# Kernel optimization log

Measured on AMD Instinct MI355X. Metric: run time of the kernel, lower is better.

The kernel has to match this reference:

```python
import jax, jax.numpy as jnp
import numpy as np

N_NODES = 100000
N_EDGES = 640000
LATDIM = 128
GNN_LAYER = 3
LN_EPS = 1e-5


def setup_inputs() -> dict:
    key = jax.random.key(0)
    k1, k2, k3, k4 = jax.random.split(key, 4)
    embeds = jax.random.normal(k1, (N_NODES, LATDIM), dtype=jnp.float32)
    adj_row = jax.random.randint(k2, (N_EDGES,), 0, N_NODES, dtype=jnp.int32)
    adj_col = jax.random.randint(k3, (N_EDGES,), 0, N_NODES, dtype=jnp.int32)
    adj_val = jax.random.uniform(k4, (N_EDGES,), dtype=jnp.float32)
    return {"embeds": embeds, "adj_row": adj_row, "adj_col": adj_col, "adj_val": adj_val}


def _layer_norm(x):
    # nn.LayerNorm(latdim, elementwise_affine=False)
    mu = jnp.mean(x, axis=-1, keepdims=True)
    var = jnp.mean(jnp.square(x - mu), axis=-1, keepdims=True)
    return (x - mu) / jnp.sqrt(var + LN_EPS)


def _spmm(adj_row, adj_col, adj_val, x):
    # out[r] += val * x[c] for each edge (r, c, val)  -- sparse [N,N] @ [N,d]
    msgs = adj_val[:, None] * x[adj_col]  # [E, d]
    return jax.ops.segment_sum(msgs, adj_row, num_segments=N_NODES)


def reference(embeds, adj_row, adj_col, adj_val):
    x = _layer_norm(embeds)
    acc = jnp.zeros_like(x)  # gnn_layer > 0, so hop-0 embeds are NOT included
    for _ in range(GNN_LAYER):
        x = _spmm(adj_row, adj_col, adj_val, x)
        acc = acc + x
    return acc
```

## Files before the change

### kernel.cpp

```cpp
#include <hip/hip_runtime.h>

#define N_NODES 100000
#define N_EDGES 640000
#define LATDIM  128
#define LN_EPS  1e-5f

typedef unsigned int u32;
typedef float f32x4 __attribute__((ext_vector_type(4)));
typedef float f32x2 __attribute__((ext_vector_type(2)));

#define SCAN_NB   98
#define N_PAD     (SCAN_NB * 1024)

#define LN_BLOCKS   (N_NODES / 8)

#define CNT_BLOCKS  100
#define CNT_K       25

#define APP_K      7
#define APP_EDGES  (256 * APP_K)
#define APP_NB     ((N_EDGES + APP_EDGES - 1) / APP_EDGES)

__device__ __forceinline__ float bflo(u32 u) { return __uint_as_float(u << 16); }
__device__ __forceinline__ float bfhi(u32 u) { return __uint_as_float(u & 0xffff0000u); }
__device__ __forceinline__ u32 pack_bf2(float a, float b) {
    u32 ua = __float_as_uint(a), ub = __float_as_uint(b);
    ua = (ua + 0x7fffu + ((ua >> 16) & 1u)) >> 16;
    ub = (ub + 0x7fffu + ((ub >> 16) & 1u)) >> 16;
    return ua | (ub << 16);
}

__device__ __forceinline__ u32 pack_edge(int col, float val) {
    u32 q = (u32)fminf(val * 32768.0f + 0.5f, 32767.0f);
    return (u32)col | (q << 17);
}
__device__ __forceinline__ int   edge_col(u32 r) { return (int)(r & 0x1FFFFu); }
__device__ __forceinline__ float edge_val(u32 r) { return (float)(r >> 17) * (1.0f / 32768.0f); }

__global__ __launch_bounds__(256) void ln_count_kernel(const float* __restrict__ in,
                                                       u32* __restrict__ out,
                                                       const int* __restrict__ rowi,
                                                       int* __restrict__ partials) {
    int b = blockIdx.x;
    if (b >= CNT_BLOCKS) {
        int tid  = threadIdx.x;
        int wave = tid >> 6;
        int lane = tid & 63;
        int half = lane >> 5;
        int sub  = lane & 31;
        int row  = (b - CNT_BLOCKS) * 8 + wave * 2 + half;
        f32x4 v = __builtin_nontemporal_load(((const f32x4*)in) + (size_t)row * 32 + sub);
        float s  = v.x + v.y + v.z + v.w;
        float ss = v.x * v.x + v.y * v.y + v.z * v.z + v.w * v.w;
        #pragma unroll
        for (int o = 16; o > 0; o >>= 1) {
            s  += __shfl_xor(s,  o, 64);
            ss += __shfl_xor(ss, o, 64);
        }
        float mu   = s * (1.0f / LATDIM);
        float var  = ss * (1.0f / LATDIM) - mu * mu;
        float rstd = rsqrtf(var + LN_EPS);
        uint2 w;
        w.x = pack_bf2((v.x - mu) * rstd, (v.y - mu) * rstd);
        w.y = pack_bf2((v.z - mu) * rstd, (v.w - mu) * rstd);
        ((uint2*)out)[(size_t)row * 32 + sub] = w;
    } else {
        __shared__ int hist[SCAN_NB];
        int t = threadIdx.x;
        if (t < SCAN_NB) hist[t] = 0;
        __syncthreads();
        int e0 = b * (256 * CNT_K);
        #pragma unroll
        for (int k = 0; k < CNT_K; ++k) {
            int e = e0 + k * 256 + t;
            atomicAdd(&hist[rowi[e] >> 10], 1);
        }
        __syncthreads();
        if (t < SCAN_NB) partials[b * SCAN_NB + t] = hist[t];
    }
}

__global__ __launch_bounds__(128) void scan_chunks_kernel(const int* __restrict__ partials,
                                                          int* __restrict__ bsums,
                                                          int* __restrict__ gcur) {
    __shared__ int ss[128];
    int t = threadIdx.x;
    int own = 0;
    if (t < SCAN_NB) {
        for (int i = 0; i < CNT_BLOCKS; ++i) own += partials[i * SCAN_NB + t];
    }
    ss[t] = own;
    __syncthreads();
    #pragma unroll
    for (int o = 1; o < 128; o <<= 1) {
        int u = 0;
        if (t >= o) u = ss[t - o];
        __syncthreads();
        if (t >= o) ss[t] += u;
        __syncthreads();
    }
    if (t < SCAN_NB) {
        int off = ss[t] - own;
        bsums[t] = off;
        gcur[t]  = off;
    }
    if (t == SCAN_NB) bsums[SCAN_NB] = N_EDGES;
}

__global__ __launch_bounds__(256) void bucket_append_kernel(const int* __restrict__ rowi,
                                                            const int* __restrict__ coli,
                                                            const float* __restrict__ vali,
                                                            int* __restrict__ gcur,
                                                            uint2* __restrict__ staging) {
    __shared__ int hist[SCAN_NB];
    __shared__ int base[SCAN_NB];
    int t = threadIdx.x;
    if (t < SCAN_NB) hist[t] = 0;
    __syncthreads();
    int e0 = blockIdx.x * APP_EDGES;
    int r[APP_K]; int c[APP_K]; float v[APP_K]; int bk[APP_K];
    #pragma unroll
    for (int k = 0; k < APP_K; ++k) {
        int e = e0 + k * 256 + t;
        if (e < N_EDGES) {
            r[k] = rowi[e]; c[k] = coli[e]; v[k] = vali[e];
            bk[k] = r[k] >> 10;
            atomicAdd(&hist[bk[k]], 1);
        } else {
            bk[k] = -1;
        }
    }
    __syncthreads();
    if (t < SCAN_NB) {
        int h = hist[t];
        base[t] = h ? atomicAdd(&gcur[t], h) : 0;
        hist[t] = 0;
    }
    __syncthreads();
    #pragma unroll
    for (int k = 0; k < APP_K; ++k) {
        if (bk[k] >= 0) {
            int idx = atomicAdd(&hist[bk[k]], 1);
            staging[base[bk[k]] + idx] =
                make_uint2(((u32)(r[k] & 1023) << 17) | (u32)c[k],
                           __float_as_uint(v[k]));
        }
    }
}

__global__ __launch_bounds__(256) void fine_scatter_kernel(int* __restrict__ cnt,
                                                           const int* __restrict__ bsums,
                                                           const uint2* __restrict__ staging,
                                                           u32* __restrict__ recs) {
    __shared__ int cur[1024];
    __shared__ int ts[256];
    int b = blockIdx.x, t = threadIdx.x;
    *(int4*)&cur[t * 4] = make_int4(0, 0, 0, 0);
    __syncthreads();
    int gbase = bsums[b];
    int n = bsums[b + 1] - gbase;
    for (int i = t; i < n; i += 256) {
        uint2 s = staging[gbase + i];
        atomicAdd(&cur[s.x >> 17], 1);
    }
    __syncthreads();
    int4 v = *(const int4*)&cur[t * 4];
    int s = v.x + v.y + v.z + v.w;
    ts[t] = s;
    __syncthreads();
    #pragma unroll
    for (int o = 1; o < 256; o <<= 1) {
        int u = 0;
        if (t >= o) u = ts[t - o];
        __syncthreads();
        if (t >= o) ts[t] += u;
        __syncthreads();
    }
    int excl = ts[t] - s;
    int4 w;
    w.x = excl;
    w.y = excl + v.x;
    w.z = excl + v.x + v.y;
    w.w = excl + v.x + v.y + v.z;
    *(int4*)&cnt[b * 1024 + t * 4] = w;
    *(int4*)&cur[t * 4] = w;
    __syncthreads();
    for (int i = t; i < n; i += 256) {
        uint2 s2 = staging[gbase + i];
        int rowLocal = (int)(s2.x >> 17);
        int col = (int)(s2.x & 0x1FFFFu);
        int pos = gbase + atomicAdd(&cur[rowLocal], 1);
        recs[pos] = pack_edge(col, __uint_as_float(s2.y));
    }
}

__global__ __launch_bounds__(256) void spmm_csr_kernel(const int* __restrict__ cnt,
                                                       const int* __restrict__ bsums,
                                                       const u32* __restrict__ recs,
                                                       const u32* __restrict__ x,
                                                       u32* __restrict__ y,
                                                       const u32* __restrict__ add0,
                                                       const u32* __restrict__ add1,
                                                       float* __restrict__ out,
                                                       int mode) {
    int tid  = threadIdx.x;
    int wave = tid >> 6;
    int lane = tid & 63;
    int row  = blockIdx.x * 4 + wave;
    int e   = cnt[row]     + bsums[row >> 10];
    int end = cnt[row + 1] + bsums[(row + 1) >> 10];
    float a0 = 0.f, a1 = 0.f;
    for (; e + 4 <= end; e += 4) {
        u32 r0 = recs[e], r1 = recs[e+1], r2 = recs[e+2], r3 = recs[e+3];
        u32 g0 = x[(size_t)edge_col(r0) * 64 + lane];
        u32 g1 = x[(size_t)edge_col(r1) * 64 + lane];
        u32 g2 = x[(size_t)edge_col(r2) * 64 + lane];
        u32 g3 = x[(size_t)edge_col(r3) * 64 + lane];
        float v0 = edge_val(r0), v1 = edge_val(r1);
        float v2 = edge_val(r2), v3 = edge_val(r3);
        a0 += v0 * bflo(g0); a1 += v0 * bfhi(g0);
        a0 += v1 * bflo(g1); a1 += v1 * bfhi(g1);
        a0 += v2 * bflo(g2); a1 += v2 * bfhi(g2);
        a0 += v3 * bflo(g3); a1 += v3 * bfhi(g3);
    }
    if (e + 2 <= end) {
        u32 r0 = recs[e], r1 = recs[e+1];
        u32 g0 = x[(size_t)edge_col(r0) * 64 + lane];
        u32 g1 = x[(size_t)edge_col(r1) * 64 + lane];
        float v0 = edge_val(r0), v1 = edge_val(r1);
        a0 += v0 * bflo(g0); a1 += v0 * bfhi(g0);
        a0 += v1 * bflo(g1); a1 += v1 * bfhi(g1);
        e += 2;
    }
    if (e < end) {
        u32 r = recs[e];
        u32 g = x[(size_t)edge_col(r) * 64 + lane];
        float v = edge_val(r);
        a0 += v * bflo(g); a1 += v * bfhi(g);
    }
    size_t oi = (size_t)row * 64 + lane;
    if (mode == 2) {
        u32 b0 = add0[oi];
        u32 b1 = add1[oi];
        a0 += bflo(b0) + bflo(b1);
        a1 += bfhi(b0) + bfhi(b1);
        f32x2 q = {a0, a1};
        __builtin_nontemporal_store(q, ((f32x2*)(out + (size_t)row * LATDIM)) + lane);
    } else {
        y[oi] = pack_bf2(a0, a1);
    }
}

__global__ __launch_bounds__(256) void ln_f32_kernel(const float* __restrict__ in,
                                                     float* __restrict__ out) {
    int tid  = threadIdx.x;
    int wave = tid >> 6;
    int lane = tid & 63;
    int half = lane >> 5;
    int sub  = lane & 31;
    int row  = blockIdx.x * 8 + wave * 2 + half;
    if (row >= N_NODES) return;
    float4 v = ((const float4*)in)[(size_t)row * 32 + sub];
    float s  = v.x + v.y + v.z + v.w;
    float ss = v.x * v.x + v.y * v.y + v.z * v.z + v.w * v.w;
    #pragma unroll
    for (int o = 16; o > 0; o >>= 1) {
        s  += __shfl_xor(s,  o, 64);
        ss += __shfl_xor(ss, o, 64);
    }
    float mu   = s * (1.0f / LATDIM);
    float var  = ss * (1.0f / LATDIM) - mu * mu;
    float rstd = rsqrtf(var + LN_EPS);
    float4 o4;
    o4.x = (v.x - mu) * rstd; o4.y = (v.y - mu) * rstd;
    o4.z = (v.z - mu) * rstd; o4.w = (v.w - mu) * rstd;
    ((float4*)out)[(size_t)row * 32 + sub] = o4;
}

__global__ __launch_bounds__(256) void spmm_atomic_kernel(const int* __restrict__ rowi,
                                                          const int* __restrict__ coli,
                                                          const float* __restrict__ vali,
                                                          const float* __restrict__ x,
                                                          float* __restrict__ y) {
    int t = blockIdx.x * 256 + threadIdx.x;
    int e = t >> 5;
    if (e >= N_EDGES) return;
    int k = t & 31;
    int r = rowi[e];
    int c = coli[e];
    float v = vali[e];
    float4 xv = ((const float4*)(x + (size_t)c * LATDIM))[k];
    float* yp = y + (size_t)r * LATDIM + k * 4;
    atomicAdd(yp + 0, v * xv.x);
    atomicAdd(yp + 1, v * xv.y);
    atomicAdd(yp + 2, v * xv.z);
    atomicAdd(yp + 3, v * xv.w);
}

__global__ __launch_bounds__(256) void addz_kernel(float* __restrict__ acc,
                                                   const float* __restrict__ x,
                                                   float* __restrict__ z,
                                                   int first) {
    size_t i = (size_t)blockIdx.x * 256 + threadIdx.x;
    float4 xv = ((const float4*)x)[i];
    float4* ap = ((float4*)acc) + i;
    if (first) {
        *ap = xv;
    } else {
        float4 a = *ap;
        a.x += xv.x; a.y += xv.y; a.z += xv.z; a.w += xv.w;
        *ap = a;
    }
    if (z) ((float4*)z)[i] = make_float4(0.f, 0.f, 0.f, 0.f);
}

extern "C" void kernel_launch(void* const* d_in, const int* in_sizes, int n_in,
                              void* d_out, int out_size, void* d_ws, size_t ws_size,
                              hipStream_t stream) {
    const float* embeds  = (const float*)d_in[0];
    const int*   adj_row = (const int*)d_in[1];
    const int*   adj_col = (const int*)d_in[2];
    const float* adj_val = (const float*)d_in[3];
    float* out = (float*)d_out;

    u32*   A16   = (u32*)d_ws;
    u32*   B16   = A16 + (size_t)N_NODES * (LATDIM / 2);
    int*   cnt   = (int*)(B16 + (size_t)N_NODES * (LATDIM / 2));
    int*   partials = cnt + N_PAD;
    int*   bsums = partials + CNT_BLOCKS * SCAN_NB;
    int*   gcur  = bsums + 128;
    uint2* staging = (uint2*)(gcur + 128);
    u32*   recs  = (u32*)(staging + N_EDGES);
    size_t need  = (size_t)((char*)(recs + N_EDGES) - (char*)d_ws);

    const int rowGrid = N_NODES / 4;

    if (ws_size >= need) {
        ln_count_kernel<<<CNT_BLOCKS + LN_BLOCKS, 256, 0, stream>>>(embeds, A16,
                                                                    adj_row, partials);
        scan_chunks_kernel<<<1, 128, 0, stream>>>(partials, bsums, gcur);
        bucket_append_kernel<<<APP_NB, 256, 0, stream>>>(adj_row, adj_col, adj_val,
                                                         gcur, staging);
        fine_scatter_kernel<<<SCAN_NB, 256, 0, stream>>>(cnt, bsums, staging, recs);
        spmm_csr_kernel<<<rowGrid, 256, 0, stream>>>(cnt, bsums, recs, A16, B16,
                                                     nullptr, nullptr, nullptr, 0);
        spmm_csr_kernel<<<rowGrid, 256, 0, stream>>>(cnt, bsums, recs, B16, A16,
                                                     nullptr, nullptr, nullptr, 0);
        spmm_csr_kernel<<<rowGrid, 256, 0, stream>>>(cnt, bsums, recs, A16, nullptr,
                                                     B16, A16, out, 2);
    } else {
        float* A = (float*)d_ws;
        float* B = A + (size_t)N_NODES * LATDIM;
        const size_t rowBytes = (size_t)N_NODES * LATDIM * sizeof(float);
        const int spmmGrid = (N_EDGES * 32 + 255) / 256;
        const int addGrid  = (N_NODES * LATDIM / 4 + 255) / 256;
        ln_f32_kernel<<<LN_BLOCKS, 256, 0, stream>>>(embeds, A);
        hipMemsetAsync(B, 0, rowBytes, stream);
        spmm_atomic_kernel<<<spmmGrid, 256, 0, stream>>>(adj_row, adj_col, adj_val, A, B);
        addz_kernel<<<addGrid, 256, 0, stream>>>(out, B, A, 1);
        spmm_atomic_kernel<<<spmmGrid, 256, 0, stream>>>(adj_row, adj_col, adj_val, B, A);
        addz_kernel<<<addGrid, 256, 0, stream>>>(out, A, B, 0);
        spmm_atomic_kernel<<<spmmGrid, 256, 0, stream>>>(adj_row, adj_col, adj_val, A, B);
        addz_kernel<<<addGrid, 256, 0, stream>>>(out, B, nullptr, 0);
    }
}
```

Before: 261.6 us.

## Process two adjacent CSR rows per 16-lane group with 16-byte gathers

The SpMM kernel now gives each 16-lane group a pair of consecutive rows, walking their combined edge range once and splitting each edge's weight between the two rows' accumulators by comparing the edge index to the row boundary. Each lane gathers a uint4 (8 bf16 values) instead of one u32, so every gathered row becomes a single 256-byte load by 16 lanes. The dequantisation scale is moved out of the loop and applied once at the end. This cuts per-edge instruction overhead and divergence from short rows, at the cost of doubled FMAs (half of them multiply by zero) and higher register pressure from 16 accumulators.

New measurement: 242.2 us. 1.08x faster.

```diff
diff --git a/kernel.cpp b/kernel.cpp
--- a/kernel.cpp
+++ b/kernel.cpp
@@ -7,7 +7,6 @@
 
 typedef unsigned int u32;
 typedef float f32x4 __attribute__((ext_vector_type(4)));
-typedef float f32x2 __attribute__((ext_vector_type(2)));
 
 #define SCAN_NB   98
 #define N_PAD     (SCAN_NB * 1024)
@@ -34,8 +33,6 @@
     u32 q = (u32)fminf(val * 32768.0f + 0.5f, 32767.0f);
     return (u32)col | (q << 17);
 }
-__device__ __forceinline__ int   edge_col(u32 r) { return (int)(r & 0x1FFFFu); }
-__device__ __forceinline__ float edge_val(u32 r) { return (float)(r >> 17) * (1.0f / 32768.0f); }
 
 __global__ __launch_bounds__(256) void ln_count_kernel(const float* __restrict__ in,
                                                        u32* __restrict__ out,
@@ -206,48 +203,115 @@
     int tid  = threadIdx.x;
     int wave = tid >> 6;
     int lane = tid & 63;
-    int row  = blockIdx.x * 4 + wave;
-    int e   = cnt[row]     + bsums[row >> 10];
-    int end = cnt[row + 1] + bsums[(row + 1) >> 10];
-    float a0 = 0.f, a1 = 0.f;
+    int rowA = blockIdx.x * 32 + wave * 8 + (lane >> 4) * 2;
+    int rowB = rowA + 1;
+    int sub  = lane & 15;
+    int e     = cnt[rowA]     + bsums[rowA >> 10];
+    int split = cnt[rowB]     + bsums[rowB >> 10];
+    int end   = cnt[rowB + 1] + bsums[(rowB + 1) >> 10];
+    const uint4* x4 = (const uint4*)x;
+    float a0=0,a1=0,a2=0,a3=0,a4=0,a5=0,a6=0,a7=0;
+    float b0=0,b1=0,b2=0,b3=0,b4=0,b5=0,b6=0,b7=0;
     for (; e + 4 <= end; e += 4) {
         u32 r0 = recs[e], r1 = recs[e+1], r2 = recs[e+2], r3 = recs[e+3];
-        u32 g0 = x[(size_t)edge_col(r0) * 64 + lane];
-        u32 g1 = x[(size_t)edge_col(r1) * 64 + lane];
-        u32 g2 = x[(size_t)edge_col(r2) * 64 + lane];
-        u32 g3 = x[(size_t)edge_col(r3) * 64 + lane];
-        float v0 = edge_val(r0), v1 = edge_val(r1);
-        float v2 = edge_val(r2), v3 = edge_val(r3);
-        a0 += v0 * bflo(g0); a1 += v0 * bfhi(g0);
-        a0 += v1 * bflo(g1); a1 += v1 * bfhi(g1);
-        a0 += v2 * bflo(g2); a1 += v2 * bfhi(g2);
-        a0 += v3 * bflo(g3); a1 += v3 * bfhi(g3);
-    }
-    if (e + 2 <= end) {
-        u32 r0 = recs[e], r1 = recs[e+1];
-        u32 g0 = x[(size_t)edge_col(r0) * 64 + lane];
-        u32 g1 = x[(size_t)edge_col(r1) * 64 + lane];
-        float v0 = edge_val(r0), v1 = edge_val(r1);
-        a0 += v0 * bflo(g0); a1 += v0 * bfhi(g0);
-        a0 += v1 * bflo(g1); a1 += v1 * bfhi(g1);
-        e += 2;
-    }
-    if (e < end) {
+        uint4 g0 = x4[(size_t)(r0 & 0x1FFFFu) * 16 + sub];
+        uint4 g1 = x4[(size_t)(r1 & 0x1FFFFu) * 16 + sub];
+        uint4 g2 = x4[(size_t)(r2 & 0x1FFFFu) * 16 + sub];
+        uint4 g3 = x4[(size_t)(r3 & 0x1FFFFu) * 16 + sub];
+        float q0 = (float)(r0 >> 17), q1 = (float)(r1 >> 17);
+        float q2 = (float)(r2 >> 17), q3 = (float)(r3 >> 17);
+        float s0 = (e + 0 < split) ? q0 : 0.f; float t0 = q0 - s0;
+        float s1 = (e + 1 < split) ? q1 : 0.f; float t1 = q1 - s1;
+        float s2 = (e + 2 < split) ? q2 : 0.f; float t2 = q2 - s2;
+        float s3 = (e + 3 < split) ? q3 : 0.f; float t3 = q3 - s3;
+        a0 += s0 * bflo(g0.x); a1 += s0 * bfhi(g0.x);
+        a2 += s0 * bflo(g0.y); a3 += s0 * bfhi(g0.y);
+        a4 += s0 * bflo(g0.z); a5 += s0 * bfhi(g0.z);
+        a6 += s0 * bflo(g0.w); a7 += s0 * bfhi(g0.w);
+        b0 += t0 * bflo(g0.x); b1 += t0 * bfhi(g0.x);
+        b2 += t0 * bflo(g0.y); b3 += t0 * bfhi(g0.y);
+        b4 += t0 * bflo(g0.z); b5 += t0 * bfhi(g0.z);
+        b6 += t0 * bflo(g0.w); b7 += t0 * bfhi(g0.w);
+        a0 += s1 * bflo(g1.x); a1 += s1 * bfhi(g1.x);
+        a2 += s1 * bflo(g1.y); a3 += s1 * bfhi(g1.y);
+        a4 += s1 * bflo(g1.z); a5 += s1 * bfhi(g1.z);
+        a6 += s1 * bflo(g1.w); a7 += s1 * bfhi(g1.w);
+        b0 += t1 * bflo(g1.x); b1 += t1 * bfhi(g1.x);
+        b2 += t1 * bflo(g1.y); b3 += t1 * bfhi(g1.y);
+        b4 += t1 * bflo(g1.z); b5 += t1 * bfhi(g1.z);
+        b6 += t1 * bflo(g1.w); b7 += t1 * bfhi(g1.w);
+        a0 += s2 * bflo(g2.x); a1 += s2 * bfhi(g2.x);
+        a2 += s2 * bflo(g2.y); a3 += s2 * bfhi(g2.y);
+        a4 += s2 * bflo(g2.z); a5 += s2 * bfhi(g2.z);
+        a6 += s2 * bflo(g2.w); a7 += s2 * bfhi(g2.w);
+        b0 += t2 * bflo(g2.x); b1 += t2 * bfhi(g2.x);
+        b2 += t2 * bflo(g2.y); b3 += t2 * bfhi(g2.y);
+        b4 += t2 * bflo(g2.z); b5 += t2 * bfhi(g2.z);
+        b6 += t2 * bflo(g2.w); b7 += t2 * bfhi(g2.w);
+        a0 += s3 * bflo(g3.x); a1 += s3 * bfhi(g3.x);
+        a2 += s3 * bflo(g3.y); a3 += s3 * bfhi(g3.y);
+        a4 += s3 * bflo(g3.z); a5 += s3 * bfhi(g3.z);
+        a6 += s3 * bflo(g3.w); a7 += s3 * bfhi(g3.w);
+        b0 += t3 * bflo(g3.x); b1 += t3 * bfhi(g3.x);
+        b2 += t3 * bflo(g3.y); b3 += t3 * bfhi(g3.y);
+        b4 += t3 * bflo(g3.z); b5 += t3 * bfhi(g3.z);
+        b6 += t3 * bflo(g3.w); b7 += t3 * bfhi(g3.w);
+    }
+    for (; e < end; ++e) {
         u32 r = recs[e];
-        u32 g = x[(size_t)edge_col(r) * 64 + lane];
-        float v = edge_val(r);
-        a0 += v * bflo(g); a1 += v * bfhi(g);
-    }
-    size_t oi = (size_t)row * 64 + lane;
+        uint4 g = x4[(size_t)(r & 0x1FFFFu) * 16 + sub];
+        float q = (float)(r >> 17);
+        float sA = (e < split) ? q : 0.f; float sB = q - sA;
+        a0 += sA * bflo(g.x); a1 += sA * bfhi(g.x);
+        a2 += sA * bflo(g.y); a3 += sA * bfhi(g.y);
+        a4 += sA * bflo(g.z); a5 += sA * bfhi(g.z);
+        a6 += sA * bflo(g.w); a7 += sA * bfhi(g.w);
+        b0 += sB * bflo(g.x); b1 += sB * bfhi(g.x);
+        b2 += sB * bflo(g.y); b3 += sB * bfhi(g.y);
+        b4 += sB * bflo(g.z); b5 += sB * bfhi(g.z);
+        b6 += sB * bflo(g.w); b7 += sB * bfhi(g.w);
+    }
+    const float sc = 1.0f / 32768.0f;
+    a0 *= sc; a1 *= sc; a2 *= sc; a3 *= sc; a4 *= sc; a5 *= sc; a6 *= sc; a7 *= sc;
+    b0 *= sc; b1 *= sc; b2 *= sc; b3 *= sc; b4 *= sc; b5 *= sc; b6 *= sc; b7 *= sc;
+    size_t oiA = (size_t)rowA * 16 + sub;
+    size_t oiB = oiA + 16;
     if (mode == 2) {
-        u32 b0 = add0[oi];
-        u32 b1 = add1[oi];
-        a0 += bflo(b0) + bflo(b1);
-        a1 += bfhi(b0) + bfhi(b1);
-        f32x2 q = {a0, a1};
-        __builtin_nontemporal_store(q, ((f32x2*)(out + (size_t)row * LATDIM)) + lane);
+        uint4 c0 = ((const uint4*)add0)[oiA];
+        uint4 c1 = ((const uint4*)add1)[oiA];
+        a0 += bflo(c0.x) + bflo(c1.x); a1 += bfhi(c0.x) + bfhi(c1.x);
+        a2 += bflo(c0.y) + bflo(c1.y); a3 += bfhi(c0.y) + bfhi(c1.y);
+        a4 += bflo(c0.z) + bflo(c1.z); a5 += bfhi(c0.z) + bfhi(c1.z);
+        a6 += bflo(c0.w) + bflo(c1.w); a7 += bfhi(c0.w) + bfhi(c1.w);
+        uint4 d0 = ((const uint4*)add0)[oiB];
+        uint4 d1 = ((const uint4*)add1)[oiB];
+        b0 += bflo(d0.x) + bflo(d1.x); b1 += bfhi(d0.x) + bfhi(d1.x);
+        b2 += bflo(d0.y) + bflo(d1.y); b3 += bfhi(d0.y) + bfhi(d1.y);
+        b4 += bflo(d0.z) + bflo(d1.z); b5 += bfhi(d0.z) + bfhi(d1.z);
+        b6 += bflo(d0.w) + bflo(d1.w); b7 += bfhi(d0.w) + bfhi(d1.w);
+        f32x4* oA = (f32x4*)(out + (size_t)rowA * LATDIM + sub * 8);
+        f32x4 qa0 = {a0, a1, a2, a3};
+        f32x4 qa1 = {a4, a5, a6, a7};
+        __builtin_nontemporal_store(qa0, oA + 0);
+        __builtin_nontemporal_store(qa1, oA + 1);
+        f32x4* oB = (f32x4*)(out + (size_t)rowB * LATDIM + sub * 8);
+        f32x4 qb0 = {b0, b1, b2, b3};
+        f32x4 qb1 = {b4, b5, b6, b7};
+        __builtin_nontemporal_store(qb0, oB + 0);
+        __builtin_nontemporal_store(qb1, oB + 1);
     } else {
-        y[oi] = pack_bf2(a0, a1);
+        uint4 wA;
+        wA.x = pack_bf2(a0, a1);
+        wA.y = pack_bf2(a2, a3);
+        wA.z = pack_bf2(a4, a5);
+        wA.w = pack_bf2(a6, a7);
+        ((uint4*)y)[oiA] = wA;
+        uint4 wB;
+        wB.x = pack_bf2(b0, b1);
+        wB.y = pack_bf2(b2, b3);
+        wB.z = pack_bf2(b4, b5);
+        wB.w = pack_bf2(b6, b7);
+        ((uint4*)y)[oiB] = wB;
     }
 }
 
@@ -333,7 +397,7 @@
     u32*   recs  = (u32*)(staging + N_EDGES);
     size_t need  = (size_t)((char*)(recs + N_EDGES) - (char*)d_ws);
 
-    const int rowGrid = N_NODES / 4;
+    const int rowGrid = N_NODES / 32;
 
     if (ws_size >= need) {
         ln_count_kernel<<<CNT_BLOCKS + LN_BLOCKS, 256, 0, stream>>>(embeds, A16,
```
